# Performance work log

Hardware: AMD Instinct MI355X
Metric: run time of the kernel (lower is better)

Reference implementation:

```python
import jax, jax.numpy as jnp
import numpy as np

SIZE = 48
DIST = 6
PAD = DIST // 2
DESIZE = SIZE - 4  # 44
CONVEY = 0.9
RATE = 5
BATCH = 4
FLAT = DESIZE * SIZE * SIZE  # 101376


def setup_inputs() -> dict:
    key = jax.random.key(0)
    ks = jax.random.split(key, 6)
    D, H, W = DESIZE, SIZE, SIZE
    return {
        "vinput": jax.random.normal(ks[0], (BATCH, D, H, W), jnp.float32),
        "frame": jax.random.normal(ks[1], (D, H, W), jnp.float32) * 0.1,
        # 0.05 scale keeps the 216-term recurrent sums ~unit magnitude over RATE steps
        "synapse": jax.random.normal(ks[2], (D, H, W, DIST, DIST, DIST), jnp.float32) * 0.05,
        "W1": jax.random.normal(ks[3], (FLAT, 1024), jnp.float32) * 0.01,
        "b1": jnp.zeros((1024,), jnp.float32),
        "W2": jax.random.normal(ks[4], (1024, 128), jnp.float32) * 0.05,
        "b2": jnp.zeros((128,), jnp.float32),
        "W3": jax.random.normal(ks[5], (128, 10), jnp.float32) * 0.1,
        "b3": jnp.zeros((10,), jnp.float32),
    }


def _local_step(neu, syn_flat, d, p):
    """Locally-connected (unshared-weight) 3D window reduce.
    neu: (B, D, H, W); syn_flat: (D, H, W, d^3).
    For each voxel, weighted sum over its d x d x d padded neighborhood."""
    B, D, H, W = neu.shape
    pad = jnp.pad(neu, ((0, 0), (p, p), (p, p), (p, p)))
    # patches: (B, d^3, D', H', W') with valid windows; keep the first D/H/W starts
    patches = jax.lax.conv_general_dilated_patches(
        pad[:, None], filter_shape=(d, d, d), window_strides=(1, 1, 1), padding="VALID"
    )
    patches = patches[:, :, :D, :H, :W]
    return jnp.einsum("bcijk,ijkc->bijk", patches, syn_flat)


def reference(vinput, frame, synapse, W1, b1, W2, b2, W3, b3):
    D, H, W = frame.shape
    d = synapse.shape[-1]
    p = d // 2
    syn_flat = synapse.reshape(D, H, W, d * d * d)
    neu = vinput + frame  # frame broadcast over batch
    for _ in range(RATE):
        out = _local_step(neu, syn_flat, d, p)
        neu = jax.nn.relu(out) * CONVEY
    x = neu.reshape(neu.shape[0], -1)
    x = jax.nn.relu(x @ W1 + b1)
    x = jax.nn.relu(x @ W2 + b2)
    return x @ W3 + b3
```

## Files before the change

kernel.cpp:

```cpp
#include <hip/hip_runtime.h>

#define SIZE   48
#define DESIZE 44
#define PAD    3
#define BATCH  4
#define FLAT   (DESIZE*SIZE*SIZE)
#define CVOL   216

#define TJ 4
#define TK 16
#define NA 6
#define NB (TJ+5)
#define NC (TK+5)
#define NEU_T (NA*NB*NC)
#define NTILE 1584
#define C4    54

#define KSLICE  96
#define NSLICES (FLAT/KSLICE)

__global__ __launch_bounds__(256) void k_synT(const float* __restrict__ syn,
                                              float* __restrict__ synT) {
    int r  = blockIdx.x;
    int i0 = r / 36;
    int r2 = r % 36;
    int j0 = (r2 / 3) * TJ;
    int k0 = (r2 % 3) * TK;
    int t  = threadIdx.x;
    float4* dst = (float4*)synT + (size_t)r * (C4 * 64);
    for (int e = t; e < C4 * 64; e += 256) {
        int c4 = e >> 6, l = e & 63;
        int dj = l >> 4, dk = l & 15;
        const float4* src = (const float4*)(syn +
            (size_t)((i0 * SIZE + j0 + dj) * SIZE + k0 + dk) * CVOL);
        dst[e] = src[c4];
    }
}

template <int CBASE, int CNT>
__device__ __forceinline__ void do_chunk4(const float4* __restrict__ sp,
                                          const float4* __restrict__ neu4,
                                          int lanebase, float acc[4]) {
    constexpr int H1n = (CNT + 1) / 2;
    constexpr int H2n = CNT - H1n;
    {
        float4 sr[H1n];
#pragma unroll
        for (int s = 0; s < H1n; ++s) sr[s] = sp[(CBASE + s) * 64];
#pragma unroll
        for (int s = 0; s < H1n; ++s) {
#pragma unroll
            for (int j = 0; j < 4; ++j) {
                const int c  = (CBASE + s) * 4 + j;
                const int off = (c / 36) * (NB * NC) + ((c % 36) / 6) * NC + (c % 6);
                const float wv = (&sr[s].x)[j];
                const float4 n4 = neu4[lanebase + off];
                acc[0] += wv * n4.x; acc[1] += wv * n4.y;
                acc[2] += wv * n4.z; acc[3] += wv * n4.w;
            }
        }
    }
    {
        float4 sr[H2n];
#pragma unroll
        for (int s = 0; s < H2n; ++s) sr[s] = sp[(CBASE + H1n + s) * 64];
#pragma unroll
        for (int s = 0; s < H2n; ++s) {
#pragma unroll
            for (int j = 0; j < 4; ++j) {
                const int c  = (CBASE + H1n + s) * 4 + j;
                const int off = (c / 36) * (NB * NC) + ((c % 36) / 6) * NC + (c % 6);
                const float wv = (&sr[s].x)[j];
                const float4 n4 = neu4[lanebase + off];
                acc[0] += wv * n4.x; acc[1] += wv * n4.y;
                acc[2] += wv * n4.z; acc[3] += wv * n4.w;
            }
        }
    }
}

template <bool FIRST>
__global__ __launch_bounds__(256, 4) void k_step(const float4* __restrict__ nin4,
                                                 const float* __restrict__ vin,
                                                 const float* __restrict__ frame,
                                                 const float* __restrict__ synT,
                                                 float4* __restrict__ nout4) {
    __shared__ float4 neu4[NEU_T];
    __shared__ float  part[4 * 256];
    int t  = threadIdx.x;
    int r  = blockIdx.x;
    int i0 = r / 36;
    int r2 = r % 36;
    int j0 = (r2 / 3) * TJ;
    int k0 = (r2 % 3) * TK;

    for (int e = t; e < NEU_T; e += 256) {
        int a   = e / (NB * NC);
        int rem = e % (NB * NC);
        int jj  = rem / NC;
        int cc  = rem % NC;
        int gi = i0 + a - PAD;
        int gj = j0 + jj - PAD;
        int gk = k0 + cc - PAD;
        float4 vv = make_float4(0.f, 0.f, 0.f, 0.f);
        if ((unsigned)gi < DESIZE && (unsigned)gj < SIZE && (unsigned)gk < SIZE) {
            int idx = (gi * SIZE + gj) * SIZE + gk;
            if (FIRST) {
                float fr = frame[idx];
                vv.x = vin[0 * FLAT + idx] + fr;
                vv.y = vin[1 * FLAT + idx] + fr;
                vv.z = vin[2 * FLAT + idx] + fr;
                vv.w = vin[3 * FLAT + idx] + fr;
            } else {
                vv = nin4[idx];
            }
        }
        neu4[e] = vv;
    }
    __syncthreads();

    int w = t >> 6, l = t & 63;
    int dj = l >> 4, dk = l & 15;
    int lanebase = dj * NC + dk;
    const float4* sp = (const float4*)synT + (size_t)r * (C4 * 64) + l;

    float acc[4] = {0.f, 0.f, 0.f, 0.f};
    switch (w) {
        case 0:  do_chunk4< 0, 14>(sp, neu4, lanebase, acc); break;
        case 1:  do_chunk4<14, 14>(sp, neu4, lanebase, acc); break;
        case 2:  do_chunk4<28, 13>(sp, neu4, lanebase, acc); break;
        default: do_chunk4<41, 13>(sp, neu4, lanebase, acc); break;
    }
#pragma unroll
    for (int bb = 0; bb < 4; ++bb) part[bb * 256 + t] = acc[bb];
    __syncthreads();

    if (t < 64) {
        float4 o;
        o.x = part[0 * 256 + t] + part[0 * 256 + 64 + t] + part[0 * 256 + 128 + t] + part[0 * 256 + 192 + t];
        o.y = part[1 * 256 + t] + part[1 * 256 + 64 + t] + part[1 * 256 + 128 + t] + part[1 * 256 + 192 + t];
        o.z = part[2 * 256 + t] + part[2 * 256 + 64 + t] + part[2 * 256 + 128 + t] + part[2 * 256 + 192 + t];
        o.w = part[3 * 256 + t] + part[3 * 256 + 64 + t] + part[3 * 256 + 128 + t] + part[3 * 256 + 192 + t];
        o.x = fmaxf(o.x, 0.f) * 0.9f;
        o.y = fmaxf(o.y, 0.f) * 0.9f;
        o.z = fmaxf(o.z, 0.f) * 0.9f;
        o.w = fmaxf(o.w, 0.f) * 0.9f;
        int dj2 = t >> 4, dk2 = t & 15;
        nout4[(i0 * SIZE + (j0 + dj2)) * SIZE + (k0 + dk2)] = o;
    }
}

__global__ __launch_bounds__(256) void k_mlp1(const float4* __restrict__ x4,
                                              const float* __restrict__ W1,
                                              float* __restrict__ partial) {
    __shared__ float xs[KSLICE * 4];
    int t = threadIdx.x;
    int s = blockIdx.x;
    int k0 = s * KSLICE;
    for (int e = t; e < KSLICE; e += 256)
        ((float4*)xs)[e] = x4[k0 + e];
    __syncthreads();
    float acc[4][4] = {};
    const float* wp = W1 + (size_t)k0 * 1024 + t * 4;
#pragma unroll 8
    for (int kk = 0; kk < KSLICE; ++kk) {
        float4 w  = *(const float4*)(wp + (size_t)kk * 1024);
        float4 xv = *(const float4*)(xs + kk * 4);
        acc[0][0] += xv.x * w.x; acc[0][1] += xv.x * w.y; acc[0][2] += xv.x * w.z; acc[0][3] += xv.x * w.w;
        acc[1][0] += xv.y * w.x; acc[1][1] += xv.y * w.y; acc[1][2] += xv.y * w.z; acc[1][3] += xv.y * w.w;
        acc[2][0] += xv.z * w.x; acc[2][1] += xv.z * w.y; acc[2][2] += xv.z * w.z; acc[2][3] += xv.z * w.w;
        acc[3][0] += xv.w * w.x; acc[3][1] += xv.w * w.y; acc[3][2] += xv.w * w.z; acc[3][3] += xv.w * w.w;
    }
#pragma unroll
    for (int b = 0; b < 4; ++b) {
        float4 o = make_float4(acc[b][0], acc[b][1], acc[b][2], acc[b][3]);
        *(float4*)(partial + (size_t)s * 4096 + b * 1024 + t * 4) = o;
    }
}

__global__ __launch_bounds__(256) void k_reduce1(const float* __restrict__ partial,
                                                 const float* __restrict__ b1,
                                                 float* __restrict__ h1) {
    __shared__ float red[16][17];
    int t = threadIdx.x;
    int e0 = blockIdx.x * 16;
    int eo = t & 15, sl = t >> 4;
    float acc = 0.f;
    for (int it = 0; it < NSLICES / 16; ++it) {
        int s = sl + 16 * it;
        acc += partial[(size_t)s * 4096 + e0 + eo];
    }
    red[sl][eo] = acc;
    __syncthreads();
    if (t < 16) {
        float a = 0.f;
#pragma unroll
        for (int rr = 0; rr < 16; ++rr) a += red[rr][t];
        int e = e0 + t;
        h1[e] = fmaxf(a + b1[e & 1023], 0.f);
    }
}

__global__ __launch_bounds__(64) void k_mlp2(const float* __restrict__ h1,
                                             const float* __restrict__ W2,
                                             float* __restrict__ partial2) {
    __shared__ float xs[32 * 4];
    int t = threadIdx.x;
    int bid = blockIdx.x;
    int s = bid >> 1, ch = bid & 1;
    int k0 = s * 32;
    for (int e = t; e < 128; e += 64) {
        int kk = e >> 2, b = e & 3;
        xs[e] = h1[b * 1024 + k0 + kk];
    }
    __syncthreads();
    float acc[4] = {0.f, 0.f, 0.f, 0.f};
    int n2 = ch * 64 + t;
#pragma unroll
    for (int kk = 0; kk < 32; ++kk) {
        float w = W2[(size_t)(k0 + kk) * 128 + n2];
        float4 xv = *(const float4*)(xs + kk * 4);
        acc[0] += xv.x * w; acc[1] += xv.y * w; acc[2] += xv.z * w; acc[3] += xv.w * w;
    }
#pragma unroll
    for (int b = 0; b < 4; ++b) partial2[s * 512 + b * 128 + n2] = acc[b];
}

__global__ __launch_bounds__(128) void k_mlp3(const float* __restrict__ partial2,
                                              const float* __restrict__ b2,
                                              const float* __restrict__ W3,
                                              const float* __restrict__ b3,
                                              float* __restrict__ out) {
    __shared__ float h2[512];
    int t = threadIdx.x;
    for (int e = t; e < 512; e += 128) {
        int n2 = e & 127;
        float a = b2[n2];
#pragma unroll 8
        for (int s = 0; s < 32; ++s) a += partial2[s * 512 + e];
        h2[e] = fmaxf(a, 0.f);
    }
    __syncthreads();
    if (t < 40) {
        int b = t / 10, o = t % 10;
        float a = b3[o];
        for (int k = 0; k < 128; ++k) a += h2[b * 128 + k] * W3[k * 10 + o];
        out[b * 10 + o] = a;
    }
}

extern "C" void kernel_launch(void* const* d_in, const int* in_sizes, int n_in,
                              void* d_out, int out_size, void* d_ws, size_t ws_size,
                              hipStream_t stream) {
    const float* vin   = (const float*)d_in[0];
    const float* frame = (const float*)d_in[1];
    const float* syn   = (const float*)d_in[2];
    const float* W1    = (const float*)d_in[3];
    const float* b1    = (const float*)d_in[4];
    const float* W2    = (const float*)d_in[5];
    const float* b2    = (const float*)d_in[6];
    const float* W3    = (const float*)d_in[7];
    const float* b3    = (const float*)d_in[8];
    float* out = (float*)d_out;

    float* ws = (float*)d_ws;
    float* A   = ws;
    float* B   = A + (size_t)BATCH * FLAT;
    float* P1  = B + (size_t)BATCH * FLAT;
    float* H1  = P1 + (size_t)NSLICES * 4096;
    float* P2  = H1 + 4096;
    float* ST  = P2 + 16384;

    k_synT<<<NTILE, 256, 0, stream>>>(syn, ST);

    k_step<true ><<<NTILE, 256, 0, stream>>>(nullptr, vin, frame, ST, (float4*)A);
    k_step<false><<<NTILE, 256, 0, stream>>>((const float4*)A, nullptr, nullptr, ST, (float4*)B);
    k_step<false><<<NTILE, 256, 0, stream>>>((const float4*)B, nullptr, nullptr, ST, (float4*)A);
    k_step<false><<<NTILE, 256, 0, stream>>>((const float4*)A, nullptr, nullptr, ST, (float4*)B);
    k_step<false><<<NTILE, 256, 0, stream>>>((const float4*)B, nullptr, nullptr, ST, (float4*)A);

    k_mlp1<<<NSLICES, 256, 0, stream>>>((const float4*)A, W1, P1);
    k_reduce1<<<256, 256, 0, stream>>>(P1, b1, H1);
    k_mlp2<<<64, 64, 0, stream>>>(H1, W2, P2);
    k_mlp3<<<1, 128, 0, stream>>>(P2, b2, W3, b3, out);
}
```

Baseline: 728.4 us.

## Fuse recurrent steps into persistent kernel with grid barrier, drop synapse transpose

Replaces the five per-step launches with one persistent kernel. Tiles are handed out dynamically through an atomic counter, and a software grid barrier sits between steps. The separate transpose pass that rearranged the synapse tensor into a coalesced per-tile layout is removed, so each lane now reads its own 216-float synapse row directly. This saves the launch gaps and one full read-and-write pass over the large synapse tensor. In exchange, the synapse loads are strided and less coalesced, and correctness depends on all 768 blocks being co-resident for the spin barrier.

```diff
diff --git a/kernel.cpp b/kernel.cpp
--- a/kernel.cpp
+++ b/kernel.cpp
@@ -14,31 +14,13 @@
 #define NC (TK+5)
 #define NEU_T (NA*NB*NC)
 #define NTILE 1584
-#define C4    54
+#define NBLK  768
 
 #define KSLICE  96
 #define NSLICES (FLAT/KSLICE)
 
-__global__ __launch_bounds__(256) void k_synT(const float* __restrict__ syn,
-                                              float* __restrict__ synT) {
-    int r  = blockIdx.x;
-    int i0 = r / 36;
-    int r2 = r % 36;
-    int j0 = (r2 / 3) * TJ;
-    int k0 = (r2 % 3) * TK;
-    int t  = threadIdx.x;
-    float4* dst = (float4*)synT + (size_t)r * (C4 * 64);
-    for (int e = t; e < C4 * 64; e += 256) {
-        int c4 = e >> 6, l = e & 63;
-        int dj = l >> 4, dk = l & 15;
-        const float4* src = (const float4*)(syn +
-            (size_t)((i0 * SIZE + j0 + dj) * SIZE + k0 + dk) * CVOL);
-        dst[e] = src[c4];
-    }
-}
-
 template <int CBASE, int CNT>
-__device__ __forceinline__ void do_chunk4(const float4* __restrict__ sp,
+__device__ __forceinline__ void do_chunk4(const float4* __restrict__ rp,
                                           const float4* __restrict__ neu4,
                                           int lanebase, float acc[4]) {
     constexpr int H1n = (CNT + 1) / 2;
@@ -46,14 +28,14 @@
     {
         float4 sr[H1n];
 #pragma unroll
-        for (int s = 0; s < H1n; ++s) sr[s] = sp[(CBASE + s) * 64];
-#pragma unroll
-        for (int s = 0; s < H1n; ++s) {
+        for (int s2 = 0; s2 < H1n; ++s2) sr[s2] = rp[CBASE + s2];
+#pragma unroll
+        for (int s2 = 0; s2 < H1n; ++s2) {
 #pragma unroll
             for (int j = 0; j < 4; ++j) {
-                const int c  = (CBASE + s) * 4 + j;
+                const int c   = (CBASE + s2) * 4 + j;
                 const int off = (c / 36) * (NB * NC) + ((c % 36) / 6) * NC + (c % 6);
-                const float wv = (&sr[s].x)[j];
+                const float wv = (&sr[s2].x)[j];
                 const float4 n4 = neu4[lanebase + off];
                 acc[0] += wv * n4.x; acc[1] += wv * n4.y;
                 acc[2] += wv * n4.z; acc[3] += wv * n4.w;
@@ -63,14 +45,14 @@
     {
         float4 sr[H2n];
 #pragma unroll
-        for (int s = 0; s < H2n; ++s) sr[s] = sp[(CBASE + H1n + s) * 64];
-#pragma unroll
-        for (int s = 0; s < H2n; ++s) {
+        for (int s2 = 0; s2 < H2n; ++s2) sr[s2] = rp[CBASE + H1n + s2];
+#pragma unroll
+        for (int s2 = 0; s2 < H2n; ++s2) {
 #pragma unroll
             for (int j = 0; j < 4; ++j) {
-                const int c  = (CBASE + H1n + s) * 4 + j;
+                const int c   = (CBASE + H1n + s2) * 4 + j;
                 const int off = (c / 36) * (NB * NC) + ((c % 36) / 6) * NC + (c % 6);
-                const float wv = (&sr[s].x)[j];
+                const float wv = (&sr[s2].x)[j];
                 const float4 n4 = neu4[lanebase + off];
                 acc[0] += wv * n4.x; acc[1] += wv * n4.y;
                 acc[2] += wv * n4.z; acc[3] += wv * n4.w;
@@ -79,74 +61,111 @@
     }
 }
 
-template <bool FIRST>
-__global__ __launch_bounds__(256, 4) void k_step(const float4* __restrict__ nin4,
-                                                 const float* __restrict__ vin,
-                                                 const float* __restrict__ frame,
-                                                 const float* __restrict__ synT,
-                                                 float4* __restrict__ nout4) {
+__device__ __forceinline__ void gbar(int* bar) {
+    __syncthreads();
+    if (threadIdx.x == 0) {
+        __threadfence();
+        int g = __hip_atomic_load(bar + 1, __ATOMIC_RELAXED, __HIP_MEMORY_SCOPE_AGENT);
+        if (atomicAdd(bar, 1) == NBLK - 1) {
+            __hip_atomic_store(bar, 0, __ATOMIC_RELAXED, __HIP_MEMORY_SCOPE_AGENT);
+            __hip_atomic_fetch_add(bar + 1, 1, __ATOMIC_RELEASE, __HIP_MEMORY_SCOPE_AGENT);
+        } else {
+            while (__hip_atomic_load(bar + 1, __ATOMIC_ACQUIRE, __HIP_MEMORY_SCOPE_AGENT) == g)
+                __builtin_amdgcn_s_sleep(2);
+        }
+        __threadfence();
+    }
+    __syncthreads();
+}
+
+__global__ void k_init(int* __restrict__ p) {
+    if (threadIdx.x < 8) p[threadIdx.x] = 0;
+}
+
+__global__ __launch_bounds__(256, 4) void k_fused(const float* __restrict__ vin,
+                                                  const float* __restrict__ frame,
+                                                  const float* __restrict__ syn,
+                                                  float4* __restrict__ A4,
+                                                  float4* __restrict__ B4,
+                                                  int* __restrict__ bar,
+                                                  int* __restrict__ ctr) {
     __shared__ float4 neu4[NEU_T];
     __shared__ float  part[4 * 256];
-    int t  = threadIdx.x;
-    int r  = blockIdx.x;
-    int i0 = r / 36;
-    int r2 = r % 36;
-    int j0 = (r2 / 3) * TJ;
-    int k0 = (r2 % 3) * TK;
-
-    for (int e = t; e < NEU_T; e += 256) {
-        int a   = e / (NB * NC);
-        int rem = e % (NB * NC);
-        int jj  = rem / NC;
-        int cc  = rem % NC;
-        int gi = i0 + a - PAD;
-        int gj = j0 + jj - PAD;
-        int gk = k0 + cc - PAD;
-        float4 vv = make_float4(0.f, 0.f, 0.f, 0.f);
-        if ((unsigned)gi < DESIZE && (unsigned)gj < SIZE && (unsigned)gk < SIZE) {
-            int idx = (gi * SIZE + gj) * SIZE + gk;
-            if (FIRST) {
-                float fr = frame[idx];
-                vv.x = vin[0 * FLAT + idx] + fr;
-                vv.y = vin[1 * FLAT + idx] + fr;
-                vv.z = vin[2 * FLAT + idx] + fr;
-                vv.w = vin[3 * FLAT + idx] + fr;
-            } else {
-                vv = nin4[idx];
+    __shared__ int    s_tile;
+    int t = threadIdx.x;
+
+    for (int s = 0; s < 5; ++s) {
+        const float4* src4 = (s & 1) ? A4 : B4;
+        float4*       dst4 = (s & 1) ? B4 : A4;
+
+        for (;;) {
+            if (t == 0) s_tile = atomicAdd(&ctr[s], 1);
+            __syncthreads();
+            int r = s_tile;
+            if (r >= NTILE) break;
+
+            int i0 = r / 36;
+            int r2 = r % 36;
+            int j0 = (r2 / 3) * TJ;
+            int k0 = (r2 % 3) * TK;
+
+            for (int e = t; e < NEU_T; e += 256) {
+                int a   = e / (NB * NC);
+                int rem = e % (NB * NC);
+                int jj  = rem / NC;
+                int cc  = rem % NC;
+                int gi = i0 + a - PAD;
+                int gj = j0 + jj - PAD;
+                int gk = k0 + cc - PAD;
+                float4 vv = make_float4(0.f, 0.f, 0.f, 0.f);
+                if ((unsigned)gi < DESIZE && (unsigned)gj < SIZE && (unsigned)gk < SIZE) {
+                    int idx = (gi * SIZE + gj) * SIZE + gk;
+                    if (s == 0) {
+                        float fr = frame[idx];
+                        vv.x = vin[0 * FLAT + idx] + fr;
+                        vv.y = vin[1 * FLAT + idx] + fr;
+                        vv.z = vin[2 * FLAT + idx] + fr;
+                        vv.w = vin[3 * FLAT + idx] + fr;
+                    } else {
+                        vv = src4[idx];
+                    }
+                }
+                neu4[e] = vv;
+            }
+            __syncthreads();
+
+            int w = t >> 6, l = t & 63;
+            int dj = l >> 4, dk = l & 15;
+            int lanebase = dj * NC + dk;
+            const float4* rp = (const float4*)(syn +
+                (size_t)((i0 * SIZE + j0 + dj) * SIZE + k0 + dk) * CVOL);
+
+            float acc[4] = {0.f, 0.f, 0.f, 0.f};
+            switch (w) {
+                case 0:  do_chunk4< 0, 14>(rp, neu4, lanebase, acc); break;
+                case 1:  do_chunk4<14, 14>(rp, neu4, lanebase, acc); break;
+                case 2:  do_chunk4<28, 13>(rp, neu4, lanebase, acc); break;
+                default: do_chunk4<41, 13>(rp, neu4, lanebase, acc); break;
+            }
+#pragma unroll
+            for (int bb = 0; bb < 4; ++bb) part[bb * 256 + t] = acc[bb];
+            __syncthreads();
+
+            if (t < 64) {
+                float4 o;
+                o.x = part[  0 + t] + part[  0 + 64 + t] + part[  0 + 128 + t] + part[  0 + 192 + t];
+                o.y = part[256 + t] + part[256 + 64 + t] + part[256 + 128 + t] + part[256 + 192 + t];
+                o.z = part[512 + t] + part[512 + 64 + t] + part[512 + 128 + t] + part[512 + 192 + t];
+                o.w = part[768 + t] + part[768 + 64 + t] + part[768 + 128 + t] + part[768 + 192 + t];
+                o.x = fmaxf(o.x, 0.f) * 0.9f;
+                o.y = fmaxf(o.y, 0.f) * 0.9f;
+                o.z = fmaxf(o.z, 0.f) * 0.9f;
+                o.w = fmaxf(o.w, 0.f) * 0.9f;
+                int dj2 = t >> 4, dk2 = t & 15;
+                dst4[(i0 * SIZE + (j0 + dj2)) * SIZE + (k0 + dk2)] = o;
             }
         }
-        neu4[e] = vv;
-    }
-    __syncthreads();
-
-    int w = t >> 6, l = t & 63;
-    int dj = l >> 4, dk = l & 15;
-    int lanebase = dj * NC + dk;
-    const float4* sp = (const float4*)synT + (size_t)r * (C4 * 64) + l;
-
-    float acc[4] = {0.f, 0.f, 0.f, 0.f};
-    switch (w) {
-        case 0:  do_chunk4< 0, 14>(sp, neu4, lanebase, acc); break;
-        case 1:  do_chunk4<14, 14>(sp, neu4, lanebase, acc); break;
-        case 2:  do_chunk4<28, 13>(sp, neu4, lanebase, acc); break;
-        default: do_chunk4<41, 13>(sp, neu4, lanebase, acc); break;
-    }
-#pragma unroll
-    for (int bb = 0; bb < 4; ++bb) part[bb * 256 + t] = acc[bb];
-    __syncthreads();
-
-    if (t < 64) {
-        float4 o;
-        o.x = part[0 * 256 + t] + part[0 * 256 + 64 + t] + part[0 * 256 + 128 + t] + part[0 * 256 + 192 + t];
-        o.y = part[1 * 256 + t] + part[1 * 256 + 64 + t] + part[1 * 256 + 128 + t] + part[1 * 256 + 192 + t];
-        o.z = part[2 * 256 + t] + part[2 * 256 + 64 + t] + part[2 * 256 + 128 + t] + part[2 * 256 + 192 + t];
-        o.w = part[3 * 256 + t] + part[3 * 256 + 64 + t] + part[3 * 256 + 128 + t] + part[3 * 256 + 192 + t];
-        o.x = fmaxf(o.x, 0.f) * 0.9f;
-        o.y = fmaxf(o.y, 0.f) * 0.9f;
-        o.z = fmaxf(o.z, 0.f) * 0.9f;
-        o.w = fmaxf(o.w, 0.f) * 0.9f;
-        int dj2 = t >> 4, dk2 = t & 15;
-        nout4[(i0 * SIZE + (j0 + dj2)) * SIZE + (k0 + dk2)] = o;
+        if (s < 4) gbar(bar);
     }
 }
 
@@ -263,21 +282,17 @@
     const float* b3    = (const float*)d_in[8];
     float* out = (float*)d_out;
 
-    float* ws = (float*)d_ws;
+    int*   ibase = (int*)d_ws;
+    float* ws    = (float*)d_ws + 16;
     float* A   = ws;
     float* B   = A + (size_t)BATCH * FLAT;
     float* P1  = B + (size_t)BATCH * FLAT;
     float* H1  = P1 + (size_t)NSLICES * 4096;
     float* P2  = H1 + 4096;
-    float* ST  = P2 + 16384;
-
-    k_synT<<<NTILE, 256, 0, stream>>>(syn, ST);
-
-    k_step<true ><<<NTILE, 256, 0, stream>>>(nullptr, vin, frame, ST, (float4*)A);
-    k_step<false><<<NTILE, 256, 0, stream>>>((const float4*)A, nullptr, nullptr, ST, (float4*)B);
-    k_step<false><<<NTILE, 256, 0, stream>>>((const float4*)B, nullptr, nullptr, ST, (float4*)A);
-    k_step<false><<<NTILE, 256, 0, stream>>>((const float4*)A, nullptr, nullptr, ST, (float4*)B);
-    k_step<false><<<NTILE, 256, 0, stream>>>((const float4*)B, nullptr, nullptr, ST, (float4*)A);
+
+    k_init<<<1, 64, 0, stream>>>(ibase);
+    k_fused<<<NBLK, 256, 0, stream>>>(vin, frame, syn,
+                                      (float4*)A, (float4*)B, ibase, ibase + 2);
 
     k_mlp1<<<NSLICES, 256, 0, stream>>>((const float4*)A, W1, P1);
     k_reduce1<<<256, 256, 0, stream>>>(P1, b1, H1);
```

Measured after the change: 1.449 ms. 99.0% more time.
